# Performance work log

Hardware: AMD Instinct MI355X
Metric: run time of the kernel (lower is better)

## Reference

```python
import jax, jax.numpy as jnp
import numpy as np


def _fo_pool(f, z):
    # c_t = f_t * c_{t-1} + z_t, c_0 = 0, scanned over axis 1 (seq).
    # Associative combine: (a1,b1) * (a2,b2) = (a1*a2, a2*b1 + b2)
    def combine(left, right):
        a1, b1 = left
        a2, b2 = right
        return a1 * a2, a2 * b1 + b2
    _, c = jax.lax.associative_scan(combine, (f, z), axis=1)
    return c


def setup_inputs() -> dict:
    key = jax.random.key(0)
    ks = jax.random.split(key, 10)
    B, S, D_in, D_model, D_mlp, n_cls = 32, 2048, 512, 1024, 1024, 128
    s = 0.02
    return {
        "x":  jax.random.normal(ks[0], (B, S, D_in), dtype=jnp.float32),
        "W":  jax.random.normal(ks[1], (D_in, 3 * D_model), dtype=jnp.float32) * s,  # Linear, bias=False
        "V":  jax.random.normal(ks[2], (D_in, 3 * D_model), dtype=jnp.float32) * s,
        "Vb": jax.random.normal(ks[3], (3 * D_model,), dtype=jnp.float32) * s,
        "W0": jax.random.normal(ks[4], (D_model, D_mlp), dtype=jnp.float32) * s,
        "b0": jax.random.normal(ks[5], (D_mlp,), dtype=jnp.float32) * s,
        "W1": jax.random.normal(ks[6], (D_mlp, D_mlp), dtype=jnp.float32) * s,
        "b1": jax.random.normal(ks[7], (D_mlp,), dtype=jnp.float32) * s,
        "W2": jax.random.normal(ks[8], (D_mlp, n_cls), dtype=jnp.float32) * s,
        "b2": jax.random.normal(ks[9], (n_cls,), dtype=jnp.float32) * s,
    }


def reference(x, W, V, Vb, W0, b0, W1, b1, W2, b2):
    # kernel_size=2 pre: W(x) + V(x shifted right by one, zero-padded)
    xprev = jnp.pad(x[:, :-1, :], ((0, 0), (1, 0), (0, 0)))  # [B,S,D_in]
    pre = jnp.einsum('bsd,dk->bsk', x, W) + jnp.einsum('bsd,dk->bsk', xprev, V) + Vb
    f, z, o = jnp.split(pre, 3, axis=-1)
    f = jax.nn.sigmoid(f)
    z = (1.0 - f) * jnp.tanh(z)
    o = jax.nn.sigmoid(o)
    c = _fo_pool(f, z)          # [B,S,D_model]
    h = c * o
    q = h[:, -1, :]             # last timestep
    # dropout is identity at inference (training=False)
    q = jax.nn.relu(q @ W0 + b0)
    q = jax.nn.relu(q @ W1 + b1)
    return q @ W2 + b2
```

## Files before the change

kernel.cpp:

```cpp
#include <hip/hip_runtime.h>
#include <cstdint>
#include <cstddef>


typedef __attribute__((ext_vector_type(8))) short short8;
typedef __attribute__((ext_vector_type(4))) float f32x4;

__device__ __forceinline__ unsigned short f2bf(float f) {
  unsigned int u = __float_as_uint(f);
  u += 0x7fffu + ((u >> 16) & 1u);
  return (unsigned short)(u >> 16);
}

__device__ __forceinline__ void gload_lds16(const void* g, void* l) {
  __builtin_amdgcn_global_load_lds(
      (const __attribute__((address_space(1))) unsigned int*)g,
      (__attribute__((address_space(3))) unsigned int*)l, 16, 0, 0);
}

__device__ __forceinline__ float sigmoidf_fast(float x) {
  return 1.f / (1.f + __expf(-x));
}
__device__ __forceinline__ float tanhf_fast(float x) {
  float a = fabsf(x);
  float e = __expf(-2.f * a);
  float t = (1.f - e) / (1.f + e);
  return copysignf(t, x);
}

__global__ void pack_x_kernel(const float* __restrict__ x, unsigned short* __restrict__ xb) {
  int gid = blockIdx.x * 256 + threadIdx.x;
  float4 v = ((const float4*)x)[gid];
  ushort4 o;
  o.x = f2bf(v.x); o.y = f2bf(v.y); o.z = f2bf(v.z); o.w = f2bf(v.w);
  ((ushort4*)xb)[gid] = o;
}

__global__ void pack_u_kernel(const float* __restrict__ W, const float* __restrict__ V,
                              unsigned short* __restrict__ U) {
  __shared__ float T[64 * 65];
  const int j0 = blockIdx.x * 64;
  const int k0 = blockIdx.y * 64;
  const int jl = threadIdx.x & 63;
  const int q  = threadIdx.x >> 6;
  const float* src = (k0 < 512) ? (W + (size_t)k0 * 3072) : (V + (size_t)(k0 - 512) * 3072);
#pragma unroll 4
  for (int i = 0; i < 16; ++i) {
    int kl = q * 16 + i;
    T[kl * 65 + jl] = src[(size_t)kl * 3072 + j0 + jl];
  }
  __syncthreads();
  const int kl = threadIdx.x & 63;
#pragma unroll 4
  for (int i = 0; i < 16; ++i) {
    int jj = q * 16 + i;
    U[(size_t)(j0 + jj) * 1024 + k0 + kl] = f2bf(T[kl * 65 + jj]);
  }
}

__global__ __launch_bounds__(512, 4) void qrnn_main(
    const unsigned short* __restrict__ xb, const float* __restrict__ xf, int use_bf,
    const unsigned short* __restrict__ U, const float* __restrict__ Vb,
    float* __restrict__ Fagg, float* __restrict__ Zagg) {
  __shared__ __align__(16) char smem[65664];
  char* As = smem;
  char* Us = smem + 32896;

  const int dt = blockIdx.x;
  const int cj = blockIdx.y;
  const int b  = blockIdx.z;
  const int tid = threadIdx.x;
  const int lane = tid & 63;
  const int wid  = tid >> 6;
  const int wm = wid >> 1, wn = wid & 1;
  const int s0 = cj * 256;

  f32x4 acc[4][4];
#pragma unroll
  for (int i = 0; i < 4; ++i)
#pragma unroll
    for (int j = 0; j < 4; ++j) acc[i][j] = f32x4{0.f, 0.f, 0.f, 0.f};

  const int mrow = wm * 64 + (lane & 15);
  const int ncol = wn * 64 + (lane & 15);
  const int rloc = lane >> 3;
  const int pc   = lane & 7;

  for (int kt = 0; kt < 8; ++kt) {
    __syncthreads();
    if (use_bf) {
#pragma unroll
      for (int p = 0; p < 4; ++p) {
        int rr = wid * 32 + p * 8 + rloc;
        int c = pc ^ (rr & 7);
        ptrdiff_t s = (ptrdiff_t)b * 2048 + (s0 - 1 + rr);
        gload_lds16(xb + s * 512 + kt * 64 + c * 8, As + (wid * 32 + p * 8) * 128);
      }
      if (tid < 8) {
        gload_lds16(xb + ((size_t)b * 2048 + s0 + 255) * 512 + kt * 64 + tid * 8,
                    As + 256 * 128);
      }
#pragma unroll
      for (int p = 0; p < 4; ++p) {
        int cc = wid * 32 + p * 8 + rloc;
        int half = cc >> 7, col = cc & 127;
        int j = (col < 64) ? (dt * 64 + col) : (1024 + dt * 64 + (col - 64));
        int c = pc ^ (cc & 7);
        gload_lds16(U + ((size_t)j << 10) + half * 512 + kt * 64 + c * 8,
                    Us + (wid * 32 + p * 8) * 128);
      }
    } else {
#pragma unroll
      for (int p = 0; p < 4; ++p) {
        int rr = (tid >> 3) + p * 64;
        int fc = tid & 7;
        int s = s0 - 1 + rr;
        uint4 v = make_uint4(0u, 0u, 0u, 0u);
        if (s >= 0) {
          const float* src = xf + (((size_t)b * 2048 + s) << 9) + kt * 64 + fc * 8;
          float4 a0 = *(const float4*)src;
          float4 a1 = *(const float4*)(src + 4);
          v.x = (unsigned)f2bf(a0.x) | ((unsigned)f2bf(a0.y) << 16);
          v.y = (unsigned)f2bf(a0.z) | ((unsigned)f2bf(a0.w) << 16);
          v.z = (unsigned)f2bf(a1.x) | ((unsigned)f2bf(a1.y) << 16);
          v.w = (unsigned)f2bf(a1.z) | ((unsigned)f2bf(a1.w) << 16);
        }
        *(uint4*)(As + rr * 128 + ((fc ^ (rr & 7)) << 4)) = v;
      }
      if (tid < 8) {
        const float* src = xf + (((size_t)b * 2048 + s0 + 255) << 9) + kt * 64 + tid * 8;
        float4 a0 = *(const float4*)src;
        float4 a1 = *(const float4*)(src + 4);
        uint4 v;
        v.x = (unsigned)f2bf(a0.x) | ((unsigned)f2bf(a0.y) << 16);
        v.y = (unsigned)f2bf(a0.z) | ((unsigned)f2bf(a0.w) << 16);
        v.z = (unsigned)f2bf(a1.x) | ((unsigned)f2bf(a1.y) << 16);
        v.w = (unsigned)f2bf(a1.z) | ((unsigned)f2bf(a1.w) << 16);
        *(uint4*)(As + 256 * 128 + (tid << 4)) = v;
      }
      {
#pragma unroll
        for (int p = 0; p < 4; ++p) {
          int cc = (tid >> 3) + p * 64;
          int half = cc >> 7, col = cc & 127;
          int j = (col < 64) ? (dt * 64 + col) : (1024 + dt * 64 + (col - 64));
          int fc = tid & 7;
          int c = fc ^ (cc & 7);
          uint4 v = *(const uint4*)(U + ((size_t)j << 10) + half * 512 + kt * 64 + c * 8);
          *(uint4*)(Us + cc * 128 + (fc << 4)) = v;
        }
      }
    }
    __syncthreads();
    if (cj == 0) {
      if (tid < 8) *(uint4*)(As + (tid << 4)) = make_uint4(0u, 0u, 0u, 0u);
      __syncthreads();
    }
#pragma unroll
    for (int h2 = 0; h2 < 2; ++h2) {
      const char* Ub = Us + h2 * 16384;
#pragma unroll
      for (int kb = 0; kb < 2; ++kb) {
        const int cbase = kb * 4 + (lane >> 4);
        short8 afr[4], bfr[4];
#pragma unroll
        for (int i = 0; i < 4; ++i) {
          int rr = mrow + i * 16 + 1 - h2;
          afr[i] = *(const short8*)(As + rr * 128 + ((cbase ^ (rr & 7)) << 4));
          int n = ncol + i * 16;
          bfr[i] = *(const short8*)(Ub + n * 128 + ((cbase ^ (n & 7)) << 4));
        }
#pragma unroll
        for (int mt = 0; mt < 4; ++mt)
#pragma unroll
          for (int nt = 0; nt < 4; ++nt)
            acc[mt][nt] = __builtin_amdgcn_mfma_f32_16x16x32_bf16(afr[mt], bfr[nt], acc[mt][nt], 0, 0, 0);
      }
    }
  }

  float* fA   = (float*)smem;
  float* tzA  = (float*)(smem + 17408);
  float* segF = (float*)(smem + 34816);
  float* segZ = (float*)(smem + 36864);

  const int d = tid & 63;
  const int dl = lane & 15;
  float vb[4];
#pragma unroll
  for (int nt = 0; nt < 4; ++nt)
    vb[nt] = Vb[wn * 1024 + dt * 64 + nt * 16 + dl];

  float F_run = 1.f, Z_run = 0.f;

  for (int ph = 0; ph < 4; ++ph) {
    __syncthreads();
    if (wm == ph) {
      float* dst = (wn == 0) ? fA : tzA;
#pragma unroll
      for (int mt = 0; mt < 4; ++mt)
#pragma unroll
        for (int nt = 0; nt < 4; ++nt)
#pragma unroll
          for (int rg = 0; rg < 4; ++rg) {
            int t = mt * 16 + ((lane >> 4) << 2) + rg;
            int c = nt * 16 + dl;
            float v = acc[mt][nt][rg] + vb[nt];
            v = (wn == 0) ? sigmoidf_fast(v) : tanhf_fast(v);
            dst[t * 68 + c] = v;
          }
    }
    __syncthreads();
    {
      int seg = tid >> 6;
      float F = 1.f, Z = 0.f;
#pragma unroll
      for (int i = 0; i < 8; ++i) {
        int t = seg * 8 + i;
        float f  = fA[t * 68 + d];
        float tz = tzA[t * 68 + d];
        float z = (1.f - f) * tz;
        Z = f * Z + z;
        F *= f;
      }
      segF[seg * 64 + d] = F;
      segZ[seg * 64 + d] = Z;
    }
    __syncthreads();
    if (tid < 64) {
#pragma unroll
      for (int sgi = 0; sgi < 8; ++sgi) {
        float Fs = segF[sgi * 64 + tid], Zs = segZ[sgi * 64 + tid];
        Z_run = Fs * Z_run + Zs;
        F_run *= Fs;
      }
    }
  }
  if (tid < 64) {
    size_t o = (((size_t)b * 8 + cj) << 10) + dt * 64 + tid;
    Fagg[o] = F_run;
    Zagg[o] = Z_run;
  }
}

__global__ void head_kernel(const float* __restrict__ x, const float* __restrict__ W,
                            const float* __restrict__ V, const float* __restrict__ Vb,
                            const float* __restrict__ Fagg, const float* __restrict__ Zagg,
                            float* __restrict__ h) {
  __shared__ float red[4][64];
  const int dl = threadIdx.x & 63;
  const int w  = threadIdx.x >> 6;
  const int d = blockIdx.x * 64 + dl;
  const int b = blockIdx.y;

  const float* xl = x + ((size_t)b * 2048 + 2047) * 512;
  const float* xp = xl - 512;
  const float* Wc = W + 2048 + d;
  const float* Vc = V + 2048 + d;
  float po = 0.f;
  const int k0 = w * 128;
#pragma unroll 8
  for (int k = k0; k < k0 + 128; ++k) {
    po += xl[k] * Wc[(size_t)k * 3072];
    po += xp[k] * Vc[(size_t)k * 3072];
  }
  red[w][dl] = po;
  __syncthreads();
  if (w == 0) {
    po = red[0][dl] + red[1][dl] + red[2][dl] + red[3][dl] + Vb[2048 + d];
    float c = 0.f;
#pragma unroll
    for (int j = 0; j < 8; ++j) {
      size_t o = (((size_t)b * 8 + j) << 10) + d;
      c = Fagg[o] * c + Zagg[o];
    }
    h[((size_t)b << 10) + d] = c * sigmoidf_fast(po);
  }
}

__global__ void init_mlp_kernel(const float* __restrict__ b0, const float* __restrict__ b1,
                                const float* __restrict__ b2,
                                float* __restrict__ q0, float* __restrict__ q1,
                                float* __restrict__ out) {
  int gid = blockIdx.x * 256 + threadIdx.x;
  q0[gid] = b0[gid & 1023];
  q1[gid] = b1[gid & 1023];
  if (gid < 4096) out[gid] = b2[gid & 127];
}

__global__ void mlp_atomic_kernel(const float* __restrict__ in, const float* __restrict__ Wt,
                                  float* __restrict__ out, int K, int N, int relu_in) {
  __shared__ float red[4][64];
  const int nl = threadIdx.x & 63;
  const int w  = threadIdx.x >> 6;
  const int n = blockIdx.x * 64 + nl;
  const int b = blockIdx.y;
  const int k0 = blockIdx.z * (K >> 2) + w * (K >> 4);
  const float* row = in + (size_t)b * K;
  const float* Wc = Wt + n;
  float s = 0.f;
#pragma unroll 8
  for (int k = k0; k < k0 + (K >> 4); ++k) {
    float v = row[k];
    if (relu_in) v = fmaxf(v, 0.f);
    s += v * Wc[(size_t)k * N];
  }
  red[w][nl] = s;
  __syncthreads();
  if (w == 0) {
    s = red[0][nl] + red[1][nl] + red[2][nl] + red[3][nl];
    atomicAdd(&out[(size_t)b * N + n], s);
  }
}

extern "C" void kernel_launch(void* const* d_in, const int* in_sizes, int n_in,
                              void* d_out, int out_size, void* d_ws, size_t ws_size,
                              hipStream_t stream) {
  const float* x  = (const float*)d_in[0];
  const float* W  = (const float*)d_in[1];
  const float* V  = (const float*)d_in[2];
  const float* Vb = (const float*)d_in[3];
  const float* W0 = (const float*)d_in[4];
  const float* b0 = (const float*)d_in[5];
  const float* W1 = (const float*)d_in[6];
  const float* b1 = (const float*)d_in[7];
  const float* W2 = (const float*)d_in[8];
  const float* b2 = (const float*)d_in[9];

  char* ws = (char*)d_ws;
  unsigned short* U = (unsigned short*)(ws);
  float* Fagg = (float*)(ws + (size_t)4 * 1024 * 1024);
  float* Zagg = (float*)(ws + (size_t)6 * 1024 * 1024);
  float* h    = (float*)(ws + (size_t)8 * 1024 * 1024);
  float* q0   = (float*)(ws + (size_t)8 * 1024 * 1024 + 256 * 1024);
  float* q1   = (float*)(ws + (size_t)8 * 1024 * 1024 + 512 * 1024);
  unsigned short* xb = (unsigned short*)(ws + (size_t)16 * 1024 * 1024);

  const size_t need_bf = (size_t)16 * 1024 * 1024 + (size_t)67108864;
  int use_bf = (ws_size >= need_bf) ? 1 : 0;

  if (use_bf) pack_x_kernel<<<32768, 256, 0, stream>>>(x, xb);
  pack_u_kernel<<<dim3(32, 16), 256, 0, stream>>>(W, V, U);
  init_mlp_kernel<<<128, 256, 0, stream>>>(b0, b1, b2, q0, q1, (float*)d_out);
  qrnn_main<<<dim3(16, 8, 32), 512, 0, stream>>>(xb, x, use_bf, U, Vb, Fagg, Zagg);
  head_kernel<<<dim3(16, 32), 256, 0, stream>>>(x, W, V, Vb, Fagg, Zagg, h);
  mlp_atomic_kernel<<<dim3(16, 32, 4), 256, 0, stream>>>(h, W0, q0, 1024, 1024, 0);
  mlp_atomic_kernel<<<dim3(16, 32, 4), 256, 0, stream>>>(q0, W1, q1, 1024, 1024, 1);
  mlp_atomic_kernel<<<dim3(2, 32, 4), 256, 0, stream>>>(q1, W2, (float*)d_out, 1024, 128, 1);
}
```

Before: 637.4 us.

## Merge prologue kernels, precompute load offsets, and redirect padded rows to zero page

```diff
diff --git a/kernel.cpp b/kernel.cpp
--- a/kernel.cpp
+++ b/kernel.cpp
@@ -5,6 +5,10 @@
 
 typedef __attribute__((ext_vector_type(8))) short short8;
 typedef __attribute__((ext_vector_type(4))) float f32x4;
+
+#define U_OFF_E    0u
+#define ZERO_OFF_E 6291456u
+#define XB_OFF_E   8388608u
 
 __device__ __forceinline__ unsigned short f2bf(float f) {
   unsigned int u = __float_as_uint(f);
@@ -28,39 +32,51 @@
   return copysignf(t, x);
 }
 
-__global__ void pack_x_kernel(const float* __restrict__ x, unsigned short* __restrict__ xb) {
-  int gid = blockIdx.x * 256 + threadIdx.x;
-  float4 v = ((const float4*)x)[gid];
-  ushort4 o;
-  o.x = f2bf(v.x); o.y = f2bf(v.y); o.z = f2bf(v.z); o.w = f2bf(v.w);
-  ((ushort4*)xb)[gid] = o;
-}
-
-__global__ void pack_u_kernel(const float* __restrict__ W, const float* __restrict__ V,
-                              unsigned short* __restrict__ U) {
+__global__ void prologue_kernel(const float* __restrict__ x, const float* __restrict__ W,
+                                const float* __restrict__ V,
+                                const float* __restrict__ b0, const float* __restrict__ b1,
+                                const float* __restrict__ b2,
+                                unsigned short* __restrict__ xb, unsigned short* __restrict__ U,
+                                float* __restrict__ q0, float* __restrict__ q1,
+                                float* __restrict__ out) {
   __shared__ float T[64 * 65];
-  const int j0 = blockIdx.x * 64;
-  const int k0 = blockIdx.y * 64;
-  const int jl = threadIdx.x & 63;
-  const int q  = threadIdx.x >> 6;
-  const float* src = (k0 < 512) ? (W + (size_t)k0 * 3072) : (V + (size_t)(k0 - 512) * 3072);
+  const int bx = blockIdx.x;
+  if (bx < 32768) {
+    int gid = bx * 256 + threadIdx.x;
+    float4 v = ((const float4*)x)[gid];
+    ushort4 o;
+    o.x = f2bf(v.x); o.y = f2bf(v.y); o.z = f2bf(v.z); o.w = f2bf(v.w);
+    ((ushort4*)xb)[gid] = o;
+  } else if (bx < 33280) {
+    const int u = bx - 32768;
+    const int j0 = (u & 31) * 64;
+    const int k0 = (u >> 5) * 64;
+    const int jl = threadIdx.x & 63;
+    const int q  = threadIdx.x >> 6;
+    const float* src = (k0 < 512) ? (W + (size_t)k0 * 3072) : (V + (size_t)(k0 - 512) * 3072);
 #pragma unroll 4
-  for (int i = 0; i < 16; ++i) {
-    int kl = q * 16 + i;
-    T[kl * 65 + jl] = src[(size_t)kl * 3072 + j0 + jl];
-  }
-  __syncthreads();
-  const int kl = threadIdx.x & 63;
+    for (int i = 0; i < 16; ++i) {
+      int kl = q * 16 + i;
+      T[kl * 65 + jl] = src[(size_t)kl * 3072 + j0 + jl];
+    }
+    __syncthreads();
+    const int kl = threadIdx.x & 63;
 #pragma unroll 4
-  for (int i = 0; i < 16; ++i) {
-    int jj = q * 16 + i;
-    U[(size_t)(j0 + jj) * 1024 + k0 + kl] = f2bf(T[kl * 65 + jj]);
+    for (int i = 0; i < 16; ++i) {
+      int jj = q * 16 + i;
+      U[(size_t)(j0 + jj) * 1024 + k0 + kl] = f2bf(T[kl * 65 + jj]);
+    }
+  } else {
+    int gid = (bx - 33280) * 256 + threadIdx.x;
+    q0[gid] = b0[gid & 1023];
+    q1[gid] = b1[gid & 1023];
+    if (gid < 4096) out[gid] = b2[gid & 127];
   }
 }
 
 __global__ __launch_bounds__(512, 4) void qrnn_main(
-    const unsigned short* __restrict__ xb, const float* __restrict__ xf, int use_bf,
-    const unsigned short* __restrict__ U, const float* __restrict__ Vb,
+    const unsigned short* __restrict__ wsb, const float* __restrict__ xf, int use_bf,
+    const float* __restrict__ Vb,
     float* __restrict__ Fagg, float* __restrict__ Zagg) {
   __shared__ __align__(16) char smem[65664];
   char* As = smem;
@@ -85,30 +101,52 @@
   const int ncol = wn * 64 + (lane & 15);
   const int rloc = lane >> 3;
   const int pc   = lane & 7;
-
+  const int c0   = lane >> 4;
+
+  unsigned voffA[4], voffU[4];
+  unsigned voffA4 = 0;
+#pragma unroll
+  for (int p = 0; p < 4; ++p) {
+    int rr = wid * 32 + p * 8 + rloc;
+    int c = pc ^ (rr & 7);
+    int sg = s0 - 1 + rr;
+    voffA[p] = (sg >= 0)
+        ? (XB_OFF_E + (unsigned)(b * 2048 + sg) * 512u + (unsigned)(c * 8))
+        : (ZERO_OFF_E + (unsigned)(pc * 8));
+    int half = rr >> 7, col = rr & 127;
+    int j = (col < 64) ? (dt * 64 + col) : (1024 + dt * 64 + (col - 64));
+    voffU[p] = (unsigned)(j * 1024 + half * 512 + c * 8);
+  }
+  if (tid < 8)
+    voffA4 = XB_OFF_E + (unsigned)(b * 2048 + s0 + 255) * 512u + (unsigned)(tid * 8);
+
+  const char* pA[2][2];
+  const char* pU[2];
+#pragma unroll
+  for (int h2 = 0; h2 < 2; ++h2) {
+    int rr = mrow + 1 - h2;
+#pragma unroll
+    for (int kb = 0; kb < 2; ++kb)
+      pA[h2][kb] = As + rr * 128 + (((kb * 4 + c0) ^ (rr & 7)) << 4);
+  }
+#pragma unroll
+  for (int kb = 0; kb < 2; ++kb)
+    pU[kb] = Us + ncol * 128 + (((kb * 4 + c0) ^ (ncol & 7)) << 4);
+
+  const unsigned short* base = wsb;
+
+#pragma unroll
   for (int kt = 0; kt < 8; ++kt) {
     __syncthreads();
     if (use_bf) {
 #pragma unroll
-      for (int p = 0; p < 4; ++p) {
-        int rr = wid * 32 + p * 8 + rloc;
-        int c = pc ^ (rr & 7);
-        ptrdiff_t s = (ptrdiff_t)b * 2048 + (s0 - 1 + rr);
-        gload_lds16(xb + s * 512 + kt * 64 + c * 8, As + (wid * 32 + p * 8) * 128);
-      }
-      if (tid < 8) {
-        gload_lds16(xb + ((size_t)b * 2048 + s0 + 255) * 512 + kt * 64 + tid * 8,
-                    As + 256 * 128);
-      }
-#pragma unroll
-      for (int p = 0; p < 4; ++p) {
-        int cc = wid * 32 + p * 8 + rloc;
-        int half = cc >> 7, col = cc & 127;
-        int j = (col < 64) ? (dt * 64 + col) : (1024 + dt * 64 + (col - 64));
-        int c = pc ^ (cc & 7);
-        gload_lds16(U + ((size_t)j << 10) + half * 512 + kt * 64 + c * 8,
-                    Us + (wid * 32 + p * 8) * 128);
-      }
+      for (int p = 0; p < 4; ++p)
+        gload_lds16(base + voffA[p], As + (wid * 32 + p * 8) * 128);
+      if (tid < 8)
+        gload_lds16(base + voffA4, As + 256 * 128);
+#pragma unroll
+      for (int p = 0; p < 4; ++p)
+        gload_lds16(base + voffU[p], Us + (wid * 32 + p * 8) * 128);
     } else {
 #pragma unroll
       for (int p = 0; p < 4; ++p) {
@@ -138,45 +176,39 @@
         v.w = (unsigned)f2bf(a1.z) | ((unsigned)f2bf(a1.w) << 16);
         *(uint4*)(As + 256 * 128 + (tid << 4)) = v;
       }
-      {
-#pragma unroll
-        for (int p = 0; p < 4; ++p) {
-          int cc = (tid >> 3) + p * 64;
-          int half = cc >> 7, col = cc & 127;
-          int j = (col < 64) ? (dt * 64 + col) : (1024 + dt * 64 + (col - 64));
-          int fc = tid & 7;
-          int c = fc ^ (cc & 7);
-          uint4 v = *(const uint4*)(U + ((size_t)j << 10) + half * 512 + kt * 64 + c * 8);
-          *(uint4*)(Us + cc * 128 + (fc << 4)) = v;
+#pragma unroll
+      for (int p = 0; p < 4; ++p) {
+        int cc = (tid >> 3) + p * 64;
+        int fc = tid & 7;
+        int c = fc ^ (cc & 7);
+        uint4 v = *(const uint4*)(wsb + voffU[0] * 0 +
+                                  (size_t)(((cc & 127) < 64 ? (dt * 64 + (cc & 127))
+                                                            : (1024 + dt * 64 + ((cc & 127) - 64)))
+                                           << 10) + (cc >> 7) * 512 + kt * 64 + c * 8);
+        *(uint4*)(Us + cc * 128 + (fc << 4)) = v;
+      }
+    }
+    __syncthreads();
+#pragma unroll
+    for (int h2 = 0; h2 < 2; ++h2) {
+#pragma unroll
+      for (int kb = 0; kb < 2; ++kb) {
+        const char* pa = pA[h2][kb];
+        const char* pu = pU[kb] + h2 * 16384;
+        short8 bfr[4];
+#pragma unroll
+        for (int nt = 0; nt < 4; ++nt)
+          bfr[nt] = *(const short8*)(pu + nt * 2048);
+#pragma unroll
+        for (int mt = 0; mt < 4; ++mt) {
+          short8 afr = *(const short8*)(pa + mt * 2048);
+#pragma unroll
+          for (int nt = 0; nt < 4; ++nt)
+            acc[mt][nt] = __builtin_amdgcn_mfma_f32_16x16x32_bf16(afr, bfr[nt], acc[mt][nt], 0, 0, 0);
         }
       }
     }
-    __syncthreads();
-    if (cj == 0) {
-      if (tid < 8) *(uint4*)(As + (tid << 4)) = make_uint4(0u, 0u, 0u, 0u);
-      __syncthreads();
-    }
-#pragma unroll
-    for (int h2 = 0; h2 < 2; ++h2) {
-      const char* Ub = Us + h2 * 16384;
-#pragma unroll
-      for (int kb = 0; kb < 2; ++kb) {
-        const int cbase = kb * 4 + (lane >> 4);
-        short8 afr[4], bfr[4];
-#pragma unroll
-        for (int i = 0; i < 4; ++i) {
-          int rr = mrow + i * 16 + 1 - h2;
-          afr[i] = *(const short8*)(As + rr * 128 + ((cbase ^ (rr & 7)) << 4));
-          int n = ncol + i * 16;
-          bfr[i] = *(const short8*)(Ub + n * 128 + ((cbase ^ (n & 7)) << 4));
-        }
-#pragma unroll
-        for (int mt = 0; mt < 4; ++mt)
-#pragma unroll
-          for (int nt = 0; nt < 4; ++nt)
-            acc[mt][nt] = __builtin_amdgcn_mfma_f32_16x16x32_bf16(afr[mt], bfr[nt], acc[mt][nt], 0, 0, 0);
-      }
-    }
+    base += 64;
   }
 
   float* fA   = (float*)smem;
@@ -276,16 +308,6 @@
     }
     h[((size_t)b << 10) + d] = c * sigmoidf_fast(po);
   }
-}
-
-__global__ void init_mlp_kernel(const float* __restrict__ b0, const float* __restrict__ b1,
-                                const float* __restrict__ b2,
-                                float* __restrict__ q0, float* __restrict__ q1,
-                                float* __restrict__ out) {
-  int gid = blockIdx.x * 256 + threadIdx.x;
-  q0[gid] = b0[gid & 1023];
-  q1[gid] = b1[gid & 1023];
-  if (gid < 4096) out[gid] = b2[gid & 127];
 }
 
 __global__ void mlp_atomic_kernel(const float* __restrict__ in, const float* __restrict__ Wt,
@@ -334,15 +356,17 @@
   float* h    = (float*)(ws + (size_t)8 * 1024 * 1024);
   float* q0   = (float*)(ws + (size_t)8 * 1024 * 1024 + 256 * 1024);
   float* q1   = (float*)(ws + (size_t)8 * 1024 * 1024 + 512 * 1024);
+  char*  zpg  = ws + (size_t)12 * 1024 * 1024;
   unsigned short* xb = (unsigned short*)(ws + (size_t)16 * 1024 * 1024);
 
   const size_t need_bf = (size_t)16 * 1024 * 1024 + (size_t)67108864;
   int use_bf = (ws_size >= need_bf) ? 1 : 0;
 
-  if (use_bf) pack_x_kernel<<<32768, 256, 0, stream>>>(x, xb);
-  pack_u_kernel<<<dim3(32, 16), 256, 0, stream>>>(W, V, U);
-  init_mlp_kernel<<<128, 256, 0, stream>>>(b0, b1, b2, q0, q1, (float*)d_out);
-  qrnn_main<<<dim3(16, 8, 32), 512, 0, stream>>>(xb, x, use_bf, U, Vb, Fagg, Zagg);
+  hipMemsetAsync(zpg, 0, 4096, stream);
+  prologue_kernel<<<33408, 256, 0, stream>>>(x, W, V, b0, b1, b2, xb, U, q0, q1,
+                                             (float*)d_out);
+  qrnn_main<<<dim3(16, 8, 32), 512, 0, stream>>>((const unsigned short*)ws, x, use_bf,
+                                                 Vb, Fagg, Zagg);
   head_kernel<<<dim3(16, 32), 256, 0, stream>>>(x, W, V, Vb, Fagg, Zagg, h);
   mlp_atomic_kernel<<<dim3(16, 32, 4), 256, 0, stream>>>(h, W0, q0, 1024, 1024, 0);
   mlp_atomic_kernel<<<dim3(16, 32, 4), 256, 0, stream>>>(q0, W1, q1, 1024, 1024, 1);
```

Result: no change. 640.8 us (+0.5%).
